# Performance work log

Measured on AMD Instinct MI355X. Metric: run time of the kernel, lower is better.

The kernel has to match this reference:

```python
import jax, jax.numpy as jnp
import numpy as np

NUM_EXPERTS = 8
N_EMBD = 1024
D_FF = 4 * N_EMBD
B, S = 4, 2048


def setup_inputs() -> dict:
    key = jax.random.key(0)
    ks = jax.random.split(key, 6)
    x = jax.random.normal(ks[0], (B, S, N_EMBD), dtype=jnp.float32)
    gate_w = jax.random.normal(ks[1], (N_EMBD, NUM_EXPERTS), dtype=jnp.float32) * 0.02
    w1 = jax.random.normal(ks[2], (NUM_EXPERTS, N_EMBD, D_FF), dtype=jnp.float32) * 0.02
    b1 = jnp.zeros((NUM_EXPERTS, D_FF), dtype=jnp.float32)
    w2 = jax.random.normal(ks[3], (NUM_EXPERTS, D_FF, N_EMBD), dtype=jnp.float32) * 0.02
    b2 = jnp.zeros((NUM_EXPERTS, N_EMBD), dtype=jnp.float32)
    return {"x": x, "gate_w": gate_w, "w1": w1, "b1": b1, "w2": w2, "b2": b2}


def reference(x, gate_w, w1, b1, w2, b2):
    Bb, Ss, D = x.shape
    x_flat = x.reshape(-1, D)                      # [T, D]
    router_logits = x_flat @ gate_w                # [T, E]
    router_probs = jax.nn.softmax(router_logits, axis=-1)
    expert_idx = jnp.argmax(router_probs, axis=-1)             # [T] int
    expert_w = jnp.take_along_axis(router_probs, expert_idx[:, None], axis=1)[:, 0]  # [T]

    out = jnp.zeros_like(x_flat)
    # fixed small loop over experts (structurally distinct weights)
    for e in range(NUM_EXPERTS):
        h = jax.nn.gelu(x_flat @ w1[e] + b1[e], approximate=False)  # [T, 4D]
        y = h @ w2[e] + b2[e]                                        # [T, D]
        sel = (expert_idx == e)
        out = out + jnp.where(sel, expert_w, 0.0)[:, None] * y
    return out.reshape(Bb, Ss, D)
```

## Files before the change

kernel.cpp:

```cpp
#include <hip/hip_runtime.h>
#include <math.h>
#include <stdint.h>

#define T_TOK  8192
#define DMODEL 1024
#define DFF    4096
#define NEXP   8
#define MAXTILES 71

static constexpr size_t OFF_COUNTS  = 0;
static constexpr size_t OFF_CURSOR  = 64;
static constexpr size_t OFF_OFFSETS = 128;
static constexpr size_t OFF_TILES   = 256;
static constexpr size_t OFF_NTILES  = 768;
static constexpr size_t OFF_EIDX    = 1024;
static constexpr size_t OFF_EW      = OFF_EIDX + (size_t)T_TOK * 4;
static constexpr size_t OFF_PERM    = OFF_EW   + (size_t)T_TOK * 4;
static constexpr size_t OFF_XB      = 131072;
static constexpr size_t OFF_W1B     = OFF_XB  + (size_t)T_TOK * DMODEL * 2;
static constexpr size_t OFF_W2B     = OFF_W1B + (size_t)NEXP * DFF * DMODEL * 2;
static constexpr size_t OFF_HB      = OFF_W2B + (size_t)NEXP * DMODEL * DFF * 2;

typedef __attribute__((ext_vector_type(8))) short short8;
typedef __attribute__((ext_vector_type(4))) float floatx4;

__device__ __forceinline__ unsigned short f2bf(float f) {
    unsigned u = __builtin_bit_cast(unsigned, f);
    u += 0x7fffu + ((u >> 16) & 1u);
    return (unsigned short)(u >> 16);
}

__device__ __forceinline__ void async16(const unsigned short* g, unsigned short* l) {
    __builtin_amdgcn_global_load_lds(
        (const __attribute__((address_space(1))) unsigned*)g,
        (__attribute__((address_space(3))) unsigned*)l, 16, 0, 0);
}

__global__ void zero_kernel(int* counts, int* cursor) {
    int t = threadIdx.x;
    if (t < NEXP) { counts[t] = 0; cursor[t] = 0; }
}

__global__ __launch_bounds__(256) void transpose_cvt_kernel(const float* __restrict__ src,
                                                            unsigned short* __restrict__ dst,
                                                            int K, int N) {
    int e  = blockIdx.z;
    int k0 = blockIdx.x * 64;
    int n0 = blockIdx.y * 64;
    const float* s = src + (size_t)e * K * N;
    unsigned short* d = dst + (size_t)e * K * N;
    __shared__ float tile[64][65];
    int tid = threadIdx.x;
    int lane16 = tid & 15, rowb = tid >> 4;
#pragma unroll
    for (int i = 0; i < 4; i++) {
        int row = i * 16 + rowb;
        float4 v = *(const float4*)(s + (size_t)(k0 + row) * N + n0 + lane16 * 4);
        tile[row][lane16 * 4 + 0] = v.x;
        tile[row][lane16 * 4 + 1] = v.y;
        tile[row][lane16 * 4 + 2] = v.z;
        tile[row][lane16 * 4 + 3] = v.w;
    }
    __syncthreads();
    int n = tid >> 2, kq = tid & 3;
#pragma unroll
    for (int h = 0; h < 2; h++) {
        int kk = (kq + h * 4) * 8;
        unsigned pk[4];
#pragma unroll
        for (int j = 0; j < 4; j++) {
            unsigned lo = f2bf(tile[kk + 2 * j][n]);
            unsigned hi = f2bf(tile[kk + 2 * j + 1][n]);
            pk[j] = lo | (hi << 16);
        }
        *(uint4*)(d + (size_t)(n0 + n) * K + k0 + kk) = *(uint4*)pk;
    }
}

__global__ __launch_bounds__(256) void router_kernel(const float* __restrict__ x,
                                                     const float* __restrict__ gw,
                                                     int* __restrict__ eidx,
                                                     float* __restrict__ ew,
                                                     unsigned short* __restrict__ xb) {
    int tid = threadIdx.x, lane = tid & 63, w = tid >> 6;
    int t = blockIdx.x * 4 + w;
    float acc[NEXP];
#pragma unroll
    for (int e = 0; e < NEXP; e++) acc[e] = 0.f;
    const float* xr = x + (size_t)t * DMODEL;
    unsigned short* xbr = xb + (size_t)t * DMODEL;
#pragma unroll
    for (int i = 0; i < 4; i++) {
        int dbase = i * 256 + lane * 4;
        float4 xv = *(const float4*)(xr + dbase);
        uint2 p;
        p.x = (unsigned)f2bf(xv.x) | ((unsigned)f2bf(xv.y) << 16);
        p.y = (unsigned)f2bf(xv.z) | ((unsigned)f2bf(xv.w) << 16);
        *(uint2*)(xbr + dbase) = p;
        float xs[4] = {xv.x, xv.y, xv.z, xv.w};
#pragma unroll
        for (int j = 0; j < 4; j++) {
            const float* gr = gw + (size_t)(dbase + j) * NEXP;
            float4 g0 = *(const float4*)(gr);
            float4 g1 = *(const float4*)(gr + 4);
            acc[0] += xs[j] * g0.x; acc[1] += xs[j] * g0.y;
            acc[2] += xs[j] * g0.z; acc[3] += xs[j] * g0.w;
            acc[4] += xs[j] * g1.x; acc[5] += xs[j] * g1.y;
            acc[6] += xs[j] * g1.z; acc[7] += xs[j] * g1.w;
        }
    }
#pragma unroll
    for (int e = 0; e < NEXP; e++) {
#pragma unroll
        for (int o = 32; o > 0; o >>= 1) acc[e] += __shfl_xor(acc[e], o, 64);
    }
    float m = acc[0]; int a = 0;
#pragma unroll
    for (int e = 1; e < NEXP; e++) { if (acc[e] > m) { m = acc[e]; a = e; } }
    float s = 0.f;
#pragma unroll
    for (int e = 0; e < NEXP; e++) s += expf(acc[e] - m);
    if (lane == 0) { eidx[t] = a; ew[t] = 1.0f / s; }
}

__global__ void hist_kernel(const int* __restrict__ eidx, int* __restrict__ counts) {
    __shared__ int lh[NEXP];
    int tid = threadIdx.x;
    if (tid < NEXP) lh[tid] = 0;
    __syncthreads();
    int e = eidx[blockIdx.x * 256 + tid];
    atomicAdd(&lh[e], 1);
    __syncthreads();
    if (tid < NEXP) atomicAdd(&counts[tid], lh[tid]);
}

__global__ void scan_kernel(const int* __restrict__ counts, int* __restrict__ offsets,
                            int* __restrict__ cursor, int* __restrict__ tiletab,
                            int* __restrict__ ntiles) {
    if (threadIdx.x == 0) {
        int s = 0, nt = 0;
        for (int e = 0; e < NEXP; e++) {
            offsets[e] = s; cursor[e] = s;
            int c = counts[e];
            int m = (c + 127) >> 7;
            for (int i = 0; i < m; i++) tiletab[nt++] = (e << 16) | i;
            s += c;
        }
        offsets[NEXP] = s;
        ntiles[0] = nt;
    }
}

__global__ void scatter_kernel(const int* __restrict__ eidx, int* __restrict__ cursor,
                               int* __restrict__ perm) {
    __shared__ int lh[NEXP];
    __shared__ int lbase[NEXP];
    int tid = threadIdx.x;
    if (tid < NEXP) lh[tid] = 0;
    __syncthreads();
    int t = blockIdx.x * 256 + tid;
    int e = eidx[t];
    int lpos = atomicAdd(&lh[e], 1);
    __syncthreads();
    if (tid < NEXP) lbase[tid] = atomicAdd(&cursor[tid], lh[tid]);
    __syncthreads();
    perm[lbase[e] + lpos] = t;
}

__global__ __launch_bounds__(256, 2) void gemm1_kernel(
    const unsigned short* __restrict__ xb,
    const unsigned short* __restrict__ w1b,
    const float* __restrict__ b1,
    const int* __restrict__ counts,
    const int* __restrict__ offsets,
    const int* __restrict__ perm,
    const int* __restrict__ tiletab,
    const int* __restrict__ ntiles,
    unsigned short* __restrict__ hb)
{
    const int ti = blockIdx.y;
    if (ti >= ntiles[0]) return;
    const int tv = tiletab[ti];
    const int e = tv >> 16, mt = tv & 0xffff, nt = blockIdx.x;
    const int cnt = counts[e];
    const int off = offsets[e];
    const int tid = threadIdx.x, lane = tid & 63, wave = tid >> 6;
    const int wm = (wave >> 1) * 64, wn = (wave & 1) * 64;
    const int lm = lane & 15, quad = lane >> 4;

    __shared__ __attribute__((aligned(16))) unsigned short As[128 * 64];
    __shared__ __attribute__((aligned(16))) unsigned short Bs[128 * 64];

    const unsigned short* a_src[4];
    const unsigned short* b_src[4];
    const int cntLoc = cnt - mt * 128;
#pragma unroll
    for (int i = 0; i < 4; i++) {
        int c = i * 256 + tid;
        int row = c >> 3;
        int g = (c & 7) ^ (row & 7);
        int r = (row < cntLoc) ? row : 0;
        int tok = perm[off + mt * 128 + r];
        a_src[i] = xb + (size_t)tok * DMODEL + g * 8;
        b_src[i] = w1b + ((size_t)e * DFF + nt * 128 + row) * DMODEL + g * 8;
    }

    floatx4 acc[4][4];
#pragma unroll
    for (int i = 0; i < 4; i++)
#pragma unroll
        for (int j = 0; j < 4; j++) acc[i][j] = floatx4{0.f, 0.f, 0.f, 0.f};

    for (int k0 = 0; k0 < DMODEL; k0 += 64) {
#pragma unroll
        for (int i = 0; i < 4; i++) {
            async16(a_src[i] + k0, &As[(i * 256 + tid) * 8]);
            async16(b_src[i] + k0, &Bs[(i * 256 + tid) * 8]);
        }
        __syncthreads();
#pragma unroll
        for (int kk = 0; kk < 2; kk++) {
            short8 af[4], bfr[4];
#pragma unroll
            for (int im = 0; im < 4; im++) {
                int m = wm + im * 16 + lm;
                int slot = (kk * 4 + quad) ^ (m & 7);
                af[im] = *(const short8*)(&As[m * 64 + slot * 8]);
            }
#pragma unroll
            for (int in = 0; in < 4; in++) {
                int n = wn + in * 16 + lm;
                int slot = (kk * 4 + quad) ^ (n & 7);
                bfr[in] = *(const short8*)(&Bs[n * 64 + slot * 8]);
            }
#pragma unroll
            for (int im = 0; im < 4; im++)
#pragma unroll
                for (int in = 0; in < 4; in++)
                    acc[im][in] = __builtin_amdgcn_mfma_f32_16x16x32_bf16(
                        af[im], bfr[in], acc[im][in], 0, 0, 0);
        }
        __syncthreads();
    }

    float b1v[4];
#pragma unroll
    for (int in = 0; in < 4; in++) b1v[in] = b1[e * DFF + nt * 128 + wn + in * 16 + lm];
#pragma unroll
    for (int im = 0; im < 4; im++) {
#pragma unroll
        for (int r = 0; r < 4; r++) {
            int row = mt * 128 + wm + im * 16 + quad * 4 + r;
            if (row < cnt) {
                size_t base = (size_t)(off + row) * DFF + nt * 128 + wn + lm;
#pragma unroll
                for (int in = 0; in < 4; in++) {
                    float v = acc[im][in][r] + b1v[in];
                    float gl = 0.5f * v * (1.0f + erff(v * 0.7071067811865475f));
                    hb[base + in * 16] = f2bf(gl);
                }
            }
        }
    }
}

__global__ __launch_bounds__(512, 4) void gemm2_kernel(
    const unsigned short* __restrict__ hb,
    const unsigned short* __restrict__ w2b,
    const float* __restrict__ b2,
    const int* __restrict__ counts,
    const int* __restrict__ offsets,
    const int* __restrict__ perm,
    const int* __restrict__ tiletab,
    const int* __restrict__ ntiles,
    const float* __restrict__ ew,
    float* __restrict__ out)
{
    const int ti = blockIdx.y;
    if (ti >= ntiles[0]) return;
    const int tv = tiletab[ti];
    const int e = tv >> 16, mt = tv & 0xffff, nt = blockIdx.x;
    const int cnt = counts[e];
    const int off = offsets[e];
    const int tid = threadIdx.x, lane = tid & 63, wave = tid >> 6;
    const int wm = (wave >> 2) * 64, wn = (wave & 3) * 32;
    const int lm = lane & 15, quad = lane >> 4;

    __shared__ __attribute__((aligned(16))) unsigned short As[128 * 64];
    __shared__ __attribute__((aligned(16))) unsigned short Bs[128 * 64];

    const unsigned short* a_src[2];
    const unsigned short* b_src[2];
#pragma unroll
    for (int i = 0; i < 2; i++) {
        int c = i * 512 + tid;
        int row = c >> 3;
        int g = (c & 7) ^ (row & 7);
        int gr = off + mt * 128 + row;
        if (gr > T_TOK - 1) gr = T_TOK - 1;
        a_src[i] = hb + (size_t)gr * DFF + g * 8;
        b_src[i] = w2b + ((size_t)e * DMODEL + nt * 128 + row) * DFF + g * 8;
    }

    floatx4 acc[4][2];
#pragma unroll
    for (int i = 0; i < 4; i++)
#pragma unroll
        for (int j = 0; j < 2; j++) acc[i][j] = floatx4{0.f, 0.f, 0.f, 0.f};

    for (int k0 = 0; k0 < DFF; k0 += 64) {
#pragma unroll
        for (int i = 0; i < 2; i++) {
            async16(a_src[i] + k0, &As[(i * 512 + tid) * 8]);
            async16(b_src[i] + k0, &Bs[(i * 512 + tid) * 8]);
        }
        __syncthreads();
#pragma unroll
        for (int kk = 0; kk < 2; kk++) {
            short8 af[4], bfr[2];
#pragma unroll
            for (int im = 0; im < 4; im++) {
                int m = wm + im * 16 + lm;
                int slot = (kk * 4 + quad) ^ (m & 7);
                af[im] = *(const short8*)(&As[m * 64 + slot * 8]);
            }
#pragma unroll
            for (int in = 0; in < 2; in++) {
                int n = wn + in * 16 + lm;
                int slot = (kk * 4 + quad) ^ (n & 7);
                bfr[in] = *(const short8*)(&Bs[n * 64 + slot * 8]);
            }
#pragma unroll
            for (int im = 0; im < 4; im++)
#pragma unroll
                for (int in = 0; in < 2; in++)
                    acc[im][in] = __builtin_amdgcn_mfma_f32_16x16x32_bf16(
                        af[im], bfr[in], acc[im][in], 0, 0, 0);
        }
        __syncthreads();
    }

    float b2v[2];
#pragma unroll
    for (int in = 0; in < 2; in++)
        b2v[in] = b2[e * DMODEL + nt * 128 + wn + in * 16 + lm];
#pragma unroll
    for (int im = 0; im < 4; im++) {
#pragma unroll
        for (int r = 0; r < 4; r++) {
            int row = mt * 128 + wm + im * 16 + quad * 4 + r;
            if (row < cnt) {
                int tok = perm[off + row];
                float wv = ew[tok];
                size_t base = (size_t)tok * DMODEL + nt * 128 + wn + lm;
#pragma unroll
                for (int in = 0; in < 2; in++)
                    out[base + in * 16] = (acc[im][in][r] + b2v[in]) * wv;
            }
        }
    }
}

extern "C" void kernel_launch(void* const* d_in, const int* in_sizes, int n_in,
                              void* d_out, int out_size, void* d_ws, size_t ws_size,
                              hipStream_t stream) {
    const float* x      = (const float*)d_in[0];
    const float* gate_w = (const float*)d_in[1];
    const float* w1     = (const float*)d_in[2];
    const float* b1     = (const float*)d_in[3];
    const float* w2     = (const float*)d_in[4];
    const float* b2     = (const float*)d_in[5];
    float* out = (float*)d_out;
    char* ws = (char*)d_ws;

    int* counts  = (int*)(ws + OFF_COUNTS);
    int* cursor  = (int*)(ws + OFF_CURSOR);
    int* offsets = (int*)(ws + OFF_OFFSETS);
    int* tiletab = (int*)(ws + OFF_TILES);
    int* ntiles  = (int*)(ws + OFF_NTILES);
    int* eidx    = (int*)(ws + OFF_EIDX);
    float* ew    = (float*)(ws + OFF_EW);
    int* perm    = (int*)(ws + OFF_PERM);
    unsigned short* xb  = (unsigned short*)(ws + OFF_XB);
    unsigned short* w1b = (unsigned short*)(ws + OFF_W1B);
    unsigned short* w2b = (unsigned short*)(ws + OFF_W2B);
    unsigned short* hb  = (unsigned short*)(ws + OFF_HB);

    zero_kernel<<<1, 64, 0, stream>>>(counts, cursor);
    {
        dim3 g(DMODEL / 64, DFF / 64, NEXP);
        transpose_cvt_kernel<<<g, 256, 0, stream>>>(w1, w1b, DMODEL, DFF);
    }
    {
        dim3 g(DFF / 64, DMODEL / 64, NEXP);
        transpose_cvt_kernel<<<g, 256, 0, stream>>>(w2, w2b, DFF, DMODEL);
    }
    router_kernel<<<T_TOK / 4, 256, 0, stream>>>(x, gate_w, eidx, ew, xb);
    hist_kernel<<<T_TOK / 256, 256, 0, stream>>>(eidx, counts);
    scan_kernel<<<1, 64, 0, stream>>>(counts, offsets, cursor, tiletab, ntiles);
    scatter_kernel<<<T_TOK / 256, 256, 0, stream>>>(eidx, cursor, perm);
    {
        dim3 g(DFF / 128, MAXTILES);
        gemm1_kernel<<<g, 256, 0, stream>>>(xb, w1b, b1, counts, offsets, perm,
                                            tiletab, ntiles, hb);
    }
    {
        dim3 g(DMODEL / 128, MAXTILES);
        gemm2_kernel<<<g, 512, 0, stream>>>(hb, w2b, b2, counts, offsets, perm,
                                            tiletab, ntiles, ew, out);
    }
}
```

Before: 583.0 us.

## Fuse histogram into router, stage gate weights in LDS, fast GELU, raise occupancy

The router kernel now transposes the gate weights into shared memory and accumulates per-expert counts with a block-local histogram, which removes the separate histogram kernel launch. The erf-based GELU in gemm1's epilogue is replaced with a sigmoid-based tanh approximation using __expf. gemm1's launch bounds are raised to allow four blocks per CU, which may force register spills. The GELU approximation slightly changes numerics relative to the exact erf form.

After: 617.1 us. +5.9%, slower.

```diff
diff --git a/kernel.cpp b/kernel.cpp
--- a/kernel.cpp
+++ b/kernel.cpp
@@ -36,6 +36,11 @@
         (__attribute__((address_space(3))) unsigned*)l, 16, 0, 0);
 }
 
+__device__ __forceinline__ float gelu_fast(float v) {
+    float u2 = v * (1.5957691216f + 0.0713548163f * v * v);
+    return v / (1.0f + __expf(-u2));
+}
+
 __global__ void zero_kernel(int* counts, int* cursor) {
     int t = threadIdx.x;
     if (t < NEXP) { counts[t] = 0; cursor[t] = 0; }
@@ -81,8 +86,30 @@
                                                      const float* __restrict__ gw,
                                                      int* __restrict__ eidx,
                                                      float* __restrict__ ew,
-                                                     unsigned short* __restrict__ xb) {
+                                                     unsigned short* __restrict__ xb,
+                                                     int* __restrict__ counts) {
+    __shared__ float gwT[NEXP][DMODEL];
+    __shared__ int lh[NEXP];
     int tid = threadIdx.x, lane = tid & 63, w = tid >> 6;
+    if (tid < NEXP) lh[tid] = 0;
+    {
+        int d0 = tid * 4;
+        const float* g = gw + (size_t)d0 * NEXP;
+        float4 a0 = *(const float4*)(g +  0), b0 = *(const float4*)(g +  4);
+        float4 a1 = *(const float4*)(g +  8), b1 = *(const float4*)(g + 12);
+        float4 a2 = *(const float4*)(g + 16), b2 = *(const float4*)(g + 20);
+        float4 a3 = *(const float4*)(g + 24), b3 = *(const float4*)(g + 28);
+        *(float4*)&gwT[0][d0] = float4{a0.x, a1.x, a2.x, a3.x};
+        *(float4*)&gwT[1][d0] = float4{a0.y, a1.y, a2.y, a3.y};
+        *(float4*)&gwT[2][d0] = float4{a0.z, a1.z, a2.z, a3.z};
+        *(float4*)&gwT[3][d0] = float4{a0.w, a1.w, a2.w, a3.w};
+        *(float4*)&gwT[4][d0] = float4{b0.x, b1.x, b2.x, b3.x};
+        *(float4*)&gwT[5][d0] = float4{b0.y, b1.y, b2.y, b3.y};
+        *(float4*)&gwT[6][d0] = float4{b0.z, b1.z, b2.z, b3.z};
+        *(float4*)&gwT[7][d0] = float4{b0.w, b1.w, b2.w, b3.w};
+    }
+    __syncthreads();
+
     int t = blockIdx.x * 4 + w;
     float acc[NEXP];
 #pragma unroll
@@ -97,16 +124,10 @@
         p.x = (unsigned)f2bf(xv.x) | ((unsigned)f2bf(xv.y) << 16);
         p.y = (unsigned)f2bf(xv.z) | ((unsigned)f2bf(xv.w) << 16);
         *(uint2*)(xbr + dbase) = p;
-        float xs[4] = {xv.x, xv.y, xv.z, xv.w};
-#pragma unroll
-        for (int j = 0; j < 4; j++) {
-            const float* gr = gw + (size_t)(dbase + j) * NEXP;
-            float4 g0 = *(const float4*)(gr);
-            float4 g1 = *(const float4*)(gr + 4);
-            acc[0] += xs[j] * g0.x; acc[1] += xs[j] * g0.y;
-            acc[2] += xs[j] * g0.z; acc[3] += xs[j] * g0.w;
-            acc[4] += xs[j] * g1.x; acc[5] += xs[j] * g1.y;
-            acc[6] += xs[j] * g1.z; acc[7] += xs[j] * g1.w;
+#pragma unroll
+        for (int e = 0; e < NEXP; e++) {
+            float4 g = *(const float4*)&gwT[e][dbase];
+            acc[e] += xv.x * g.x + xv.y * g.y + xv.z * g.z + xv.w * g.w;
         }
     }
 #pragma unroll
@@ -120,18 +141,9 @@
     float s = 0.f;
 #pragma unroll
     for (int e = 0; e < NEXP; e++) s += expf(acc[e] - m);
-    if (lane == 0) { eidx[t] = a; ew[t] = 1.0f / s; }
-}
-
-__global__ void hist_kernel(const int* __restrict__ eidx, int* __restrict__ counts) {
-    __shared__ int lh[NEXP];
-    int tid = threadIdx.x;
-    if (tid < NEXP) lh[tid] = 0;
-    __syncthreads();
-    int e = eidx[blockIdx.x * 256 + tid];
-    atomicAdd(&lh[e], 1);
-    __syncthreads();
-    if (tid < NEXP) atomicAdd(&counts[tid], lh[tid]);
+    if (lane == 0) { eidx[t] = a; ew[t] = 1.0f / s; atomicAdd(&lh[a], 1); }
+    __syncthreads();
+    if (tid < NEXP && lh[tid]) atomicAdd(&counts[tid], lh[tid]);
 }
 
 __global__ void scan_kernel(const int* __restrict__ counts, int* __restrict__ offsets,
@@ -167,7 +179,7 @@
     perm[lbase[e] + lpos] = t;
 }
 
-__global__ __launch_bounds__(256, 2) void gemm1_kernel(
+__global__ __launch_bounds__(256, 4) void gemm1_kernel(
     const unsigned short* __restrict__ xb,
     const unsigned short* __restrict__ w1b,
     const float* __restrict__ b1,
@@ -256,8 +268,7 @@
 #pragma unroll
                 for (int in = 0; in < 4; in++) {
                     float v = acc[im][in][r] + b1v[in];
-                    float gl = 0.5f * v * (1.0f + erff(v * 0.7071067811865475f));
-                    hb[base + in * 16] = f2bf(gl);
+                    hb[base + in * 16] = f2bf(gelu_fast(v));
                 }
             }
         }
@@ -395,8 +406,7 @@
         dim3 g(DFF / 64, DMODEL / 64, NEXP);
         transpose_cvt_kernel<<<g, 256, 0, stream>>>(w2, w2b, DFF, DMODEL);
     }
-    router_kernel<<<T_TOK / 4, 256, 0, stream>>>(x, gate_w, eidx, ew, xb);
-    hist_kernel<<<T_TOK / 256, 256, 0, stream>>>(eidx, counts);
+    router_kernel<<<T_TOK / 4, 256, 0, stream>>>(x, gate_w, eidx, ew, xb, counts);
     scan_kernel<<<1, 64, 0, stream>>>(counts, offsets, cursor, tiletab, ntiles);
     scatter_kernel<<<T_TOK / 256, 256, 0, stream>>>(eidx, cursor, perm);
     {
```
